# Kernel optimization log

Measured on AMD Instinct MI355X. Metric: run time of the kernel, lower is better.

The kernel has to match this reference:

```python
import jax, jax.numpy as jnp
import numpy as np


def setup_inputs() -> dict:
    key = jax.random.key(0)
    k1, k2, k3 = jax.random.split(key, 3)
    B, T, D, Uh = 64, 256, 1024, 1024
    x = jax.random.normal(k1, (B, T, D), dtype=jnp.float32)
    W = jax.random.normal(k2, (D, 4 * Uh), dtype=jnp.float32) * 0.02
    U = jax.random.normal(k3, (Uh, 4 * Uh), dtype=jnp.float32) * 0.02
    b = jnp.zeros((4 * Uh,), dtype=jnp.float32)
    return {"x": x, "W": W, "U": U, "b": b}


def _lstm(x, W, U, b):
    # Keras LSTM, inference mode (dropout inactive). Gate order: i, f, c, o.
    B = x.shape[0]
    units = U.shape[0]
    # Precompute input projection for all timesteps: [B,T,4U] -> scan over T.
    xz = jnp.einsum('btd,dg->btg', x, W) + b
    xz = jnp.swapaxes(xz, 0, 1)  # [T,B,4U]

    def step(carry, xz_t):
        h, c = carry
        z = xz_t + h @ U  # [B,4U]
        zi, zf, zg, zo = jnp.split(z, 4, axis=-1)
        i = jax.nn.sigmoid(zi)
        f = jax.nn.sigmoid(zf)
        g = jnp.tanh(zg)
        o = jax.nn.sigmoid(zo)
        c_new = f * c + i * g
        h_new = o * jnp.tanh(c_new)
        return (h_new, c_new), h_new

    h0 = jnp.zeros((B, units), dtype=x.dtype)
    c0 = jnp.zeros((B, units), dtype=x.dtype)
    _, hs = jax.lax.scan(step, (h0, c0), xz)  # hs: [T,B,U]
    return jnp.swapaxes(hs, 0, 1)  # [B,T,U] (return_sequences=True)


def reference(x, W, U, b):
    return _lstm(x, W, U, b)
```

## Files before the change

### kernel.cpp

```cpp
#include <hip/hip_runtime.h>
#include <cstdint>
#include <cstddef>

typedef __attribute__((ext_vector_type(8))) short short8;
typedef __attribute__((ext_vector_type(4))) short short4v;
typedef __attribute__((ext_vector_type(4))) float f32x4;
typedef __attribute__((ext_vector_type(4))) int int4v;

static constexpr int B_ = 64, T_ = 256, D_ = 1024, NH = 1024, NG = 4096;
static constexpr int NBLK = 64;
static constexpr int LDS_BYTES = 131072 + 64 * 68 * 4;
static constexpr int GEMM_LDS = 128 * 264 * 2;
static constexpr uint64_t DLY_TICKS = 50;

__device__ __forceinline__ short f2bs(float f) {
  union { float f; uint32_t u; } cv; cv.f = f;
  uint32_t u = cv.u;
  uint32_t r = (u + 0x7fffu + ((u >> 16) & 1u)) >> 16;
  return (short)(uint16_t)r;
}
__device__ __forceinline__ float bs2f(short s) {
  union { uint32_t u; float f; } cv; cv.u = ((uint32_t)(uint16_t)s) << 16; return cv.f;
}
__device__ __forceinline__ float fsigm(float x) {
  return __builtin_amdgcn_rcpf(1.f + __expf(-x));
}
__device__ __forceinline__ float ftanh(float x) {
  return 1.f - 2.f * __builtin_amdgcn_rcpf(__expf(2.f * x) + 1.f);
}
__device__ __forceinline__ uint64_t rtclock() {
  uint64_t v;
  asm volatile("s_memrealtime %0\n\ts_waitcnt lgkmcnt(0)" : "=s"(v));
  return v;
}

__global__ __launch_bounds__(512, 1) void xz_gemm(const float* __restrict__ x,
                                                  const float* __restrict__ W,
                                                  const float* __restrict__ bias,
                                                  short* __restrict__ xzT)
{
  constexpr int BM = 256, BN = 256, BK = 32;
  extern __shared__ char gsm[];
  short* As = (short*)gsm;
  short* Bs = (short*)(gsm + 16384);
  short* Cs = (short*)gsm;

  const int tid  = threadIdx.x;
  const int lane = tid & 63, wave = tid >> 6;
  const int wm = (wave >> 2) * 128, wn = (wave & 3) * 64;
  const int fr = lane & 15, kg = lane >> 4;
  const int bm = blockIdx.x * BM, bn = blockIdx.y * BN;

  f32x4 acc[8][4] = {};

  for (int k0 = 0; k0 < D_; k0 += BK) {
    {
      const int r0 = tid >> 3, kq = (tid & 7) * 4;
      #pragma unroll
      for (int it = 0; it < 4; ++it) {
        const int row = r0 + it * 64;
        const float4 v = *reinterpret_cast<const float4*>(&x[(size_t)(bm + row) * D_ + k0 + kq]);
        short4v s; s.x = f2bs(v.x); s.y = f2bs(v.y); s.z = f2bs(v.z); s.w = f2bs(v.w);
        *reinterpret_cast<short4v*>(&As[row * 32 + kq]) = s;
      }
    }
    {
      const int kr0 = tid >> 6, nq = (tid & 63) * 4;
      #pragma unroll
      for (int it = 0; it < 4; ++it) {
        const int krow = kr0 + it * 8;
        const float4 v = *reinterpret_cast<const float4*>(&W[(size_t)(k0 + krow) * NG + bn + nq]);
        short4v s; s.x = f2bs(v.x); s.y = f2bs(v.y); s.z = f2bs(v.z); s.w = f2bs(v.w);
        *reinterpret_cast<short4v*>(&Bs[krow * 256 + nq]) = s;
      }
    }
    __syncthreads();

    short8 af[8];
    #pragma unroll
    for (int mi = 0; mi < 8; ++mi)
      af[mi] = *reinterpret_cast<const short8*>(&As[(wm + mi * 16 + fr) * 32 + kg * 8]);
    #pragma unroll
    for (int ni = 0; ni < 4; ++ni) {
      short8 bf;
      #pragma unroll
      for (int j = 0; j < 8; ++j) bf[j] = Bs[(kg * 8 + j) * 256 + wn + ni * 16 + fr];
      #pragma unroll
      for (int mi = 0; mi < 8; ++mi)
        acc[mi][ni] = __builtin_amdgcn_mfma_f32_16x16x32_bf16(af[mi], bf, acc[mi][ni], 0, 0, 0);
    }
    __syncthreads();
  }

  const int fq = lane >> 4;
  const int b   = blockIdx.x;
  const int g   = bn >> 10;
  const int rb0 = (bn & 1023) >> 4;
  #pragma unroll
  for (int hp = 0; hp < 2; ++hp) {
    __syncthreads();
    if ((wave >> 2) == hp) {
      #pragma unroll
      for (int ni = 0; ni < 4; ++ni) {
        const int col = wn + ni * 16 + fr;
        const float bv = bias[bn + col];
        #pragma unroll
        for (int mi = 0; mi < 8; ++mi) {
          const int rowl = mi * 16 + fq * 4;
          #pragma unroll
          for (int r = 0; r < 4; ++r)
            Cs[(rowl + r) * 264 + col] = f2bs(acc[mi][ni][r] + bv);
        }
      }
    }
    __syncthreads();
    #pragma unroll
    for (int it = 0; it < 4; ++it) {
      const int cid = it * 512 + tid;
      const int tl = cid >> 4, rbi = cid & 15;
      const int t = hp * 128 + tl;
      short* dst = xzT + ((size_t)((rb0 + rbi) * 256 + t) * 64 + b) * 64 + g * 16;
      const short8 v0 = *reinterpret_cast<const short8*>(&Cs[tl * 264 + rbi * 16]);
      const short8 v1 = *reinterpret_cast<const short8*>(&Cs[tl * 264 + rbi * 16 + 8]);
      *reinterpret_cast<short8*>(dst)     = v0;
      *reinterpret_cast<short8*>(dst + 8) = v1;
    }
  }
}

#define WAITV(N) do { asm volatile("s_waitcnt vmcnt(" #N ")" ::: "memory"); \
                      __builtin_amdgcn_sched_barrier(0); } while (0)

#define HL2(B0, B1, VO) \
  asm volatile("global_load_dwordx4 %0, %2, %3 sc0 sc1\n\t" \
               "global_load_dwordx4 %1, %2, %3 offset:16 sc0 sc1" \
               : "=&v"(B0), "=&v"(B1) : "v"(VO), "s"(hpv) : "memory")

#define ISSUE_A { _Pragma("unroll") \
  for (int K = 0; K < 8; ++K) HL2(bufA[2*K], bufA[2*K+1], voff0 + K * 8192); }
#define ISSUE_B { _Pragma("unroll") \
  for (int K = 0; K < 8; ++K) HL2(bufB[2*K], bufB[2*K+1], voff0 + 65536 + K * 8192); }

#define CHECKBUF(BUF) { _Pragma("unroll") \
  for (int i = 0; i < 16; ++i) { \
    bad |= ((uint32_t)BUF[i][0] ^ tgw); bad |= ((uint32_t)BUF[i][1] ^ tgw); \
    bad |= ((uint32_t)BUF[i][2] ^ tgw); bad |= ((uint32_t)BUF[i][3] ^ tgw); \
  } bad &= 0xFFFF0000u; }

#define MFMA_SUB(BUF, KB) { _Pragma("unroll") \
  for (int K = 0; K < 8; ++K) { \
    int4v pk; \
    pk[0] = (BUF[2*K][0]   & 0xFFFF) | (BUF[2*K][1]   << 16); \
    pk[1] = (BUF[2*K][2]   & 0xFFFF) | (BUF[2*K][3]   << 16); \
    pk[2] = (BUF[2*K+1][0] & 0xFFFF) | (BUF[2*K+1][1] << 16); \
    pk[3] = (BUF[2*K+1][2] & 0xFFFF) | (BUF[2*K+1][3] << 16); \
    const short8 fa = __builtin_bit_cast(short8, pk); \
    const int ksAbs = kh * 16 + (KB) + K; \
    _Pragma("unroll") \
    for (int nt = 0; nt < 4; ++nt) { \
      const short8 fb = *reinterpret_cast<const short8*>(&Us[((ksAbs*4 + kg)*64 + nt*16 + fr)*8]); \
      acc[nt] = __builtin_amdgcn_mfma_f32_16x16x32_bf16(fa, fb, acc[nt], 0, 0, 0); \
    } \
  } }

__global__ __launch_bounds__(512, 2) void lstm_persist(const short* __restrict__ xzT,
                                                       const float* __restrict__ U,
                                                       uint32_t* __restrict__ h0buf,
                                                       uint32_t* __restrict__ h1buf,
                                                       float* __restrict__ out)
{
  extern __shared__ char smem[];
  short* Us  = (short*)smem;
  float* zsm = (float*)(smem + 131072);

  const int tid  = threadIdx.x;
  const int lane = tid & 63, wave = tid >> 6;
  const int bid  = blockIdx.x;
  const int u0   = bid * 16;
  const int fr = lane & 15, kg = lane >> 4;
  const int mt = wave & 3;
  const int kh = wave >> 2;
  const int gb = tid >> 3, gup = tid & 7;

  for (int idx = tid; idx < 1024 * 64; idx += 512) {
    const int k = idx >> 6, c = idx & 63;
    Us[((k >> 3) * 64 + c) * 8 + (k & 7)] =
        f2bs(U[(size_t)k * NG + (c >> 4) * NH + u0 + (c & 15)]);
  }
  float creg0 = 0.f, creg1 = 0.f;
  const int voff0 = kh * 131072 + kg * 2048 + mt * 512 + fr * 32;
  const int pks = bid >> 1;
  const int pkg = ((bid & 1) << 1) + (gup >> 2);
  const int pj  = (2 * gup) & 7;
  const int pidx = ((pks * 4 + pkg) * 64 + gb) * 8 + pj;
  __syncthreads();
  uint64_t rt0 = rtclock();

  for (int t = 0; t < T_; ++t) {
    const uint32_t* __restrict__ hpv = (t & 1) ? h0buf : h1buf;
    uint32_t* __restrict__ hnx       = (t & 1) ? h1buf : h0buf;

    int xzw[4];
    {
      const short* xb = xzT + (((size_t)bid * 256 + t) * 64 + gb) * 64;
      #pragma unroll
      for (int g = 0; g < 4; ++g)
        xzw[g] = *reinterpret_cast<const int*>(xb + g * 16 + 2 * gup);
    }

    f32x4 acc[4] = {};
    if (t > 0) {
      const uint32_t tgw = (uint32_t)t << 16;
      int4v bufA[16], bufB[16];
      while ((uint64_t)(rtclock() - rt0) < DLY_TICKS)
        __builtin_amdgcn_s_sleep(1);
      ISSUE_A; ISSUE_B;
      WAITV(16);
      for (;;) {
        uint32_t bad = 0; CHECKBUF(bufA);
        if (__all(bad == 0)) break;
        __builtin_amdgcn_s_sleep(4);
        ISSUE_A; WAITV(0);
      }
      MFMA_SUB(bufA, 0);
      WAITV(0);
      for (;;) {
        uint32_t bad = 0; CHECKBUF(bufB);
        if (__all(bad == 0)) break;
        __builtin_amdgcn_s_sleep(4);
        ISSUE_B; WAITV(0);
      }
      MFMA_SUB(bufB, 8);

      if (kh == 1) {
        #pragma unroll
        for (int nt = 0; nt < 4; ++nt)
          #pragma unroll
          for (int r = 0; r < 4; ++r)
            zsm[(mt * 16 + kg * 4 + r) * 68 + nt * 16 + fr] = acc[nt][r];
      }
      __syncthreads();
      if (kh == 0) {
        #pragma unroll
        for (int nt = 0; nt < 4; ++nt)
          #pragma unroll
          for (int r = 0; r < 4; ++r)
            zsm[(mt * 16 + kg * 4 + r) * 68 + nt * 16 + fr] += acc[nt][r];
      }
      __syncthreads();
    }

    {
      float z[4][2];
      #pragma unroll
      for (int g = 0; g < 4; ++g) {
        z[g][0] = bs2f((short)(xzw[g] & 0xFFFF));
        z[g][1] = bs2f((short)(((uint32_t)xzw[g]) >> 16));
        if (t > 0) {
          const float2 zz = *reinterpret_cast<const float2*>(&zsm[gb * 68 + g * 16 + 2 * gup]);
          z[g][0] += zz.x; z[g][1] += zz.y;
        }
      }
      float hh0, hh1;
      {
        const float ig = fsigm(z[0][0]), fg = fsigm(z[1][0]);
        const float gg = ftanh(z[2][0]), og = fsigm(z[3][0]);
        creg0 = fg * creg0 + ig * gg;  hh0 = og * ftanh(creg0);
      }
      {
        const float ig = fsigm(z[0][1]), fg = fsigm(z[1][1]);
        const float gg = ftanh(z[2][1]), og = fsigm(z[3][1]);
        creg1 = fg * creg1 + ig * gg;  hh1 = og * ftanh(creg1);
      }
      if (t < T_ - 1) {
        const uint32_t tgp = (uint32_t)(t + 1) << 16;
        const uint64_t hw64 =
            (uint64_t)(tgp | (uint32_t)(uint16_t)f2bs(hh0)) |
            ((uint64_t)(tgp | (uint32_t)(uint16_t)f2bs(hh1)) << 32);
        (void)__hip_atomic_exchange((uint64_t*)(hnx + pidx), hw64,
                                    __ATOMIC_RELAXED, __HIP_MEMORY_SCOPE_AGENT);
      }
      rt0 = rtclock();
      float2 o; o.x = hh0; o.y = hh1;
      *reinterpret_cast<float2*>(&out[((size_t)gb * T_ + t) * NH + u0 + 2 * gup]) = o;
    }
    __builtin_amdgcn_s_barrier();
  }
}

extern "C" void kernel_launch(void* const* d_in, const int* in_sizes, int n_in,
                              void* d_out, int out_size, void* d_ws, size_t ws_size,
                              hipStream_t stream) {
  const float* x    = (const float*)d_in[0];
  const float* W    = (const float*)d_in[1];
  const float* U    = (const float*)d_in[2];
  const float* bias = (const float*)d_in[3];
  float* out = (float*)d_out;
  char* ws = (char*)d_ws;

  short*    xzT = (short*)ws;
  uint32_t* hA  = (uint32_t*)(ws + 134217728);
  uint32_t* hB  = (uint32_t*)(ws + 134217728 + 262144);

  hipMemsetAsync(ws + 134217728, 0, 524288, stream);

  hipFuncSetAttribute((const void*)xz_gemm,
                      hipFuncAttributeMaxDynamicSharedMemorySize, GEMM_LDS);
  xz_gemm<<<dim3(64, 16), 512, GEMM_LDS, stream>>>(x, W, bias, xzT);

  hipFuncSetAttribute((const void*)lstm_persist,
                      hipFuncAttributeMaxDynamicSharedMemorySize, LDS_BYTES);
  lstm_persist<<<dim3(NBLK), dim3(512), LDS_BYTES, stream>>>(xzT, U, hA, hB, out);
}
```

Before: 1.954 ms.

## Rewrite recurrent LSTM kernel with int8 weights and hidden state across 256 blocks

Replaces the 64-block persistent recurrence with a 256-block kernel. Work is split into 8 batch groups times 32 unit slices. U is quantized to int8 with per-column scales and h to int8, so the per-step matmul uses i8 MFMA with a smaller A operand. The xz layout and the h exchange buffers are reorganized for the new decomposition, and the realtime-clock delay is replaced by retry polling with cache-bypass escalation. This aims to cut per-step latency and spread the work across more CUs, at the cost of int8 quantization error on both weights and the hidden state.

```diff
diff --git a/kernel.cpp b/kernel.cpp
--- a/kernel.cpp
+++ b/kernel.cpp
@@ -6,12 +6,11 @@
 typedef __attribute__((ext_vector_type(4))) short short4v;
 typedef __attribute__((ext_vector_type(4))) float f32x4;
 typedef __attribute__((ext_vector_type(4))) int int4v;
+typedef __attribute__((ext_vector_type(2))) int int2v;
 
 static constexpr int B_ = 64, T_ = 256, D_ = 1024, NH = 1024, NG = 4096;
-static constexpr int NBLK = 64;
-static constexpr int LDS_BYTES = 131072 + 64 * 68 * 4;
 static constexpr int GEMM_LDS = 128 * 264 * 2;
-static constexpr uint64_t DLY_TICKS = 50;
+static constexpr int REC_LDS = 131072 + 4352 + 512 + 2048;
 
 __device__ __forceinline__ short f2bs(float f) {
   union { float f; uint32_t u; } cv; cv.f = f;
@@ -27,11 +26,6 @@
 }
 __device__ __forceinline__ float ftanh(float x) {
   return 1.f - 2.f * __builtin_amdgcn_rcpf(__expf(2.f * x) + 1.f);
-}
-__device__ __forceinline__ uint64_t rtclock() {
-  uint64_t v;
-  asm volatile("s_memrealtime %0\n\ts_waitcnt lgkmcnt(0)" : "=s"(v));
-  return v;
 }
 
 __global__ __launch_bounds__(512, 1) void xz_gemm(const float* __restrict__ x,
@@ -93,9 +87,9 @@
   }
 
   const int fq = lane >> 4;
-  const int b   = blockIdx.x;
-  const int g   = bn >> 10;
-  const int rb0 = (bn & 1023) >> 4;
+  const int bglob = blockIdx.x;
+  const int gg    = bn >> 10;
+  const int utile = bn & 1023;
   #pragma unroll
   for (int hp = 0; hp < 2; ++hp) {
     __syncthreads();
@@ -119,7 +113,11 @@
       const int cid = it * 512 + tid;
       const int tl = cid >> 4, rbi = cid & 15;
       const int t = hp * 128 + tl;
-      short* dst = xzT + ((size_t)((rb0 + rbi) * 256 + t) * 64 + b) * 64 + g * 16;
+      const int ul = utile + rbi * 16;
+      const int slc = ul >> 5, ub = ul & 31;
+      const int bidr = slc * 8 + (bglob >> 3);
+      short* dst = xzT + (size_t)bidr * 262144 + (size_t)t * 1024
+                 + (bglob & 7) * 128 + gg * 32 + ub;
       const short8 v0 = *reinterpret_cast<const short8*>(&Cs[tl * 264 + rbi * 16]);
       const short8 v1 = *reinterpret_cast<const short8*>(&Cs[tl * 264 + rbi * 16 + 8]);
       *reinterpret_cast<short8*>(dst)     = v0;
@@ -131,158 +129,158 @@
 #define WAITV(N) do { asm volatile("s_waitcnt vmcnt(" #N ")" ::: "memory"); \
                       __builtin_amdgcn_sched_barrier(0); } while (0)
 
-#define HL2(B0, B1, VO) \
-  asm volatile("global_load_dwordx4 %0, %2, %3 sc0 sc1\n\t" \
-               "global_load_dwordx4 %1, %2, %3 offset:16 sc0 sc1" \
-               : "=&v"(B0), "=&v"(B1) : "v"(VO), "s"(hpv) : "memory")
-
-#define ISSUE_A { _Pragma("unroll") \
-  for (int K = 0; K < 8; ++K) HL2(bufA[2*K], bufA[2*K+1], voff0 + K * 8192); }
-#define ISSUE_B { _Pragma("unroll") \
-  for (int K = 0; K < 8; ++K) HL2(bufB[2*K], bufB[2*K+1], voff0 + 65536 + K * 8192); }
-
-#define CHECKBUF(BUF) { _Pragma("unroll") \
+#define H1F(B0, VO) \
+  asm volatile("global_load_dwordx4 %0, %1, %2 sc0" \
+               : "=&v"(B0) : "v"(VO), "s"(hpv) : "memory")
+#define H1S(B0, VO) \
+  asm volatile("global_load_dwordx4 %0, %1, %2 sc0 sc1" \
+               : "=&v"(B0) : "v"(VO), "s"(hpv) : "memory")
+
+#define ISSUE16F(BUF, BASE) { _Pragma("unroll") \
+  for (int K = 0; K < 16; ++K) H1F(BUF[K], voff0 + (BASE) + K * 1024); }
+#define ISSUE16S(BUF, BASE) { _Pragma("unroll") \
+  for (int K = 0; K < 16; ++K) H1S(BUF[K], voff0 + (BASE) + K * 1024); }
+
+#define CHECK16(BUF) { uint32_t bb = 0; _Pragma("unroll") \
   for (int i = 0; i < 16; ++i) { \
-    bad |= ((uint32_t)BUF[i][0] ^ tgw); bad |= ((uint32_t)BUF[i][1] ^ tgw); \
-    bad |= ((uint32_t)BUF[i][2] ^ tgw); bad |= ((uint32_t)BUF[i][3] ^ tgw); \
-  } bad &= 0xFFFF0000u; }
-
-#define MFMA_SUB(BUF, KB) { _Pragma("unroll") \
-  for (int K = 0; K < 8; ++K) { \
-    int4v pk; \
-    pk[0] = (BUF[2*K][0]   & 0xFFFF) | (BUF[2*K][1]   << 16); \
-    pk[1] = (BUF[2*K][2]   & 0xFFFF) | (BUF[2*K][3]   << 16); \
-    pk[2] = (BUF[2*K+1][0] & 0xFFFF) | (BUF[2*K+1][1] << 16); \
-    pk[3] = (BUF[2*K+1][2] & 0xFFFF) | (BUF[2*K+1][3] << 16); \
-    const short8 fa = __builtin_bit_cast(short8, pk); \
-    const int ksAbs = kh * 16 + (KB) + K; \
-    _Pragma("unroll") \
-    for (int nt = 0; nt < 4; ++nt) { \
-      const short8 fb = *reinterpret_cast<const short8*>(&Us[((ksAbs*4 + kg)*64 + nt*16 + fr)*8]); \
-      acc[nt] = __builtin_amdgcn_mfma_f32_16x16x32_bf16(fa, fb, acc[nt], 0, 0, 0); \
-    } \
+    bb |= ((uint32_t)BUF[i][0] ^ tgw); bb |= ((uint32_t)BUF[i][1] ^ tgw); \
+    bb |= ((uint32_t)BUF[i][2] ^ tgw); bb |= ((uint32_t)BUF[i][3] ^ tgw); \
+  } bad = frlt8 ? (bb & 0xFFFF0000u) : 0u; }
+
+#define MFMA16(BUF, KB) { _Pragma("unroll") \
+  for (int K = 0; K < 16; ++K) { \
+    int2v ad; \
+    ad[0] = (BUF[K][0] & 0xFFFF) | ((BUF[K][1] & 0xFFFF) << 16); \
+    ad[1] = (BUF[K][2] & 0xFFFF) | ((BUF[K][3] & 0xFFFF) << 16); \
+    const long long a64 = frlt8 ? __builtin_bit_cast(long long, ad) : 0ll; \
+    const int ksAbs = (KB) + K; \
+    const long long b64 = *reinterpret_cast<const long long*>( \
+        &Us[(size_t)(((ksAbs * 4 + kg) * 128 + wave * 16 + fr)) * 8]); \
+    acc = __builtin_amdgcn_mfma_i32_16x16x32_i8(a64, b64, acc, 0, 0, 0); \
   } }
 
-__global__ __launch_bounds__(512, 2) void lstm_persist(const short* __restrict__ xzT,
-                                                       const float* __restrict__ U,
-                                                       uint32_t* __restrict__ h0buf,
-                                                       uint32_t* __restrict__ h1buf,
-                                                       float* __restrict__ out)
+__global__ __launch_bounds__(512, 2) void lstm_rec(
+    const short* __restrict__ xzT, const float* __restrict__ U,
+    uint32_t* __restrict__ h0buf, uint32_t* __restrict__ h1buf,
+    float* __restrict__ out)
 {
   extern __shared__ char smem[];
-  short* Us  = (short*)smem;
-  float* zsm = (float*)(smem + 131072);
+  char*  Us   = smem;
+  float* zsm  = (float*)(smem + 131072);
+  float* scl  = (float*)(smem + 131072 + 4352);
+  float* pmax = (float*)(smem + 131072 + 4864);
 
   const int tid  = threadIdx.x;
   const int lane = tid & 63, wave = tid >> 6;
   const int bid  = blockIdx.x;
-  const int u0   = bid * 16;
+  const int g    = bid & 7;
+  const int sl   = bid >> 3;
   const int fr = lane & 15, kg = lane >> 4;
-  const int mt = wave & 3;
-  const int kh = wave >> 2;
-  const int gb = tid >> 3, gup = tid & 7;
-
-  for (int idx = tid; idx < 1024 * 64; idx += 512) {
-    const int k = idx >> 6, c = idx & 63;
-    Us[((k >> 3) * 64 + c) * 8 + (k & 7)] =
-        f2bs(U[(size_t)k * NG + (c >> 4) * NH + u0 + (c & 15)]);
-  }
-  float creg0 = 0.f, creg1 = 0.f;
-  const int voff0 = kh * 131072 + kg * 2048 + mt * 512 + fr * 32;
-  const int pks = bid >> 1;
-  const int pkg = ((bid & 1) << 1) + (gup >> 2);
-  const int pj  = (2 * gup) & 7;
-  const int pidx = ((pks * 4 + pkg) * 64 + gb) * 8 + pj;
+  const bool frlt8 = (fr < 8);
+
+  {
+    const int c = tid & 127, q = tid >> 7;
+    const float* up = U + (size_t)(q * 256) * NG + (c >> 5) * NH + sl * 32 + (c & 31);
+    float m = 1e-30f;
+    for (int k = 0; k < 256; ++k) m = fmaxf(m, fabsf(up[(size_t)k * NG]));
+    pmax[q * 128 + c] = m;
+  }
   __syncthreads();
-  uint64_t rt0 = rtclock();
+  if (tid < 128)
+    scl[tid] = fmaxf(fmaxf(pmax[tid], pmax[128 + tid]),
+                     fmaxf(pmax[256 + tid], pmax[384 + tid]));
+  __syncthreads();
+  for (int idx = tid; idx < 131072; idx += 512) {
+    const int k = idx >> 7, c = idx & 127;
+    const float v = U[(size_t)k * NG + (c >> 5) * NH + sl * 32 + (c & 31)];
+    Us[(size_t)(((k >> 5) * 4 + ((k >> 3) & 3)) * 128 + c) * 8 + (k & 7)] =
+        (char)(int)rintf(v * (127.f / scl[c]));
+  }
+  const float sdiv = scl[wave * 16 + fr] * (1.f / 16129.f);
+  float creg = 0.f;
+  const int voff0 = kg * 256 + fr * 16;
+  __syncthreads();
 
   for (int t = 0; t < T_; ++t) {
-    const uint32_t* __restrict__ hpv = (t & 1) ? h0buf : h1buf;
-    uint32_t* __restrict__ hnx       = (t & 1) ? h1buf : h0buf;
-
-    int xzw[4];
-    {
-      const short* xb = xzT + (((size_t)bid * 256 + t) * 64 + gb) * 64;
-      #pragma unroll
-      for (int g = 0; g < 4; ++g)
-        xzw[g] = *reinterpret_cast<const int*>(xb + g * 16 + 2 * gup);
-    }
-
-    f32x4 acc[4] = {};
+    const uint32_t* hpv = ((t & 1) ? h0buf : h1buf) + g * 8192;
+    uint32_t*       hnx = ((t & 1) ? h1buf : h0buf) + g * 8192;
+
+    float xzv0 = 0.f, xzv1 = 0.f, xzv2 = 0.f, xzv3 = 0.f;
+    if (tid < 256) {
+      const short* xb = xzT + (size_t)bid * 262144 + (size_t)t * 1024
+                      + (tid >> 5) * 128 + (tid & 31);
+      xzv0 = bs2f(xb[0]);  xzv1 = bs2f(xb[32]);
+      xzv2 = bs2f(xb[64]); xzv3 = bs2f(xb[96]);
+    }
+
+    int4v acc = {};
     if (t > 0) {
       const uint32_t tgw = (uint32_t)t << 16;
       int4v bufA[16], bufB[16];
-      while ((uint64_t)(rtclock() - rt0) < DLY_TICKS)
-        __builtin_amdgcn_s_sleep(1);
-      ISSUE_A; ISSUE_B;
+      if (frlt8) { ISSUE16F(bufA, 0); ISSUE16F(bufB, 16384); }
       WAITV(16);
-      for (;;) {
-        uint32_t bad = 0; CHECKBUF(bufA);
-        if (__all(bad == 0)) break;
-        __builtin_amdgcn_s_sleep(4);
-        ISSUE_A; WAITV(0);
-      }
-      MFMA_SUB(bufA, 0);
+      {
+        int tries = 0; uint32_t bad;
+        for (;;) {
+          CHECK16(bufA);
+          if (__all(bad == 0)) break;
+          __builtin_amdgcn_s_sleep(1);
+          ++tries;
+          if (frlt8) { if (tries < 6) { ISSUE16F(bufA, 0); } else { ISSUE16S(bufA, 0); } }
+          WAITV(0);
+        }
+      }
+      MFMA16(bufA, 0);
       WAITV(0);
-      for (;;) {
-        uint32_t bad = 0; CHECKBUF(bufB);
-        if (__all(bad == 0)) break;
-        __builtin_amdgcn_s_sleep(4);
-        ISSUE_B; WAITV(0);
-      }
-      MFMA_SUB(bufB, 8);
-
-      if (kh == 1) {
+      {
+        int tries = 0; uint32_t bad;
+        for (;;) {
+          CHECK16(bufB);
+          if (__all(bad == 0)) break;
+          __builtin_amdgcn_s_sleep(1);
+          ++tries;
+          if (frlt8) { if (tries < 6) { ISSUE16F(bufB, 16384); } else { ISSUE16S(bufB, 16384); } }
+          WAITV(0);
+        }
+      }
+      MFMA16(bufB, 16);
+
+      if (lane < 32) {
+        const int rowb = (lane >> 4) * 4;
         #pragma unroll
-        for (int nt = 0; nt < 4; ++nt)
-          #pragma unroll
-          for (int r = 0; r < 4; ++r)
-            zsm[(mt * 16 + kg * 4 + r) * 68 + nt * 16 + fr] = acc[nt][r];
-      }
-      __syncthreads();
-      if (kh == 0) {
-        #pragma unroll
-        for (int nt = 0; nt < 4; ++nt)
-          #pragma unroll
-          for (int r = 0; r < 4; ++r)
-            zsm[(mt * 16 + kg * 4 + r) * 68 + nt * 16 + fr] += acc[nt][r];
-      }
-      __syncthreads();
-    }
-
-    {
-      float z[4][2];
-      #pragma unroll
-      for (int g = 0; g < 4; ++g) {
-        z[g][0] = bs2f((short)(xzw[g] & 0xFFFF));
-        z[g][1] = bs2f((short)(((uint32_t)xzw[g]) >> 16));
-        if (t > 0) {
-          const float2 zz = *reinterpret_cast<const float2*>(&zsm[gb * 68 + g * 16 + 2 * gup]);
-          z[g][0] += zz.x; z[g][1] += zz.y;
+        for (int r = 0; r < 4; ++r)
+          zsm[(rowb + r) * 132 + wave * 16 + fr] = (float)acc[r] * sdiv;
+      }
+    }
+    __syncthreads();
+
+    if (tid < 256) {
+      const int b = tid >> 5, uu = tid & 31;
+      float z0 = xzv0, z1 = xzv1, z2 = xzv2, z3 = xzv3;
+      if (t > 0) {
+        z0 += zsm[b * 132 + uu];
+        z1 += zsm[b * 132 + 32 + uu];
+        z2 += zsm[b * 132 + 64 + uu];
+        z3 += zsm[b * 132 + 96 + uu];
+      }
+      const float ig = fsigm(z0), fg = fsigm(z1);
+      const float gg2 = ftanh(z2), og = fsigm(z3);
+      creg = fg * creg + ig * gg2;
+      const float hh = og * ftanh(creg);
+
+      if (t < T_ - 1) {
+        const int q = (int)rintf(hh * 127.f);
+        const int qp = __shfl_xor(q, 1);
+        if (!(uu & 1)) {
+          const uint32_t word = ((uint32_t)(t + 1) << 16)
+                              | (((uint32_t)qp & 0xFFu) << 8) | ((uint32_t)q & 0xFFu);
+          uint32_t* hp = hnx + ((sl * 4 + (uu >> 3)) * 16 + b) * 4 + ((uu >> 1) & 3);
+          asm volatile("global_store_dword %0, %1, off sc0\n\t"
+                       "global_store_dword %0, %1, off sc0 sc1"
+                       :: "v"(hp), "v"(word) : "memory");
         }
       }
-      float hh0, hh1;
-      {
-        const float ig = fsigm(z[0][0]), fg = fsigm(z[1][0]);
-        const float gg = ftanh(z[2][0]), og = fsigm(z[3][0]);
-        creg0 = fg * creg0 + ig * gg;  hh0 = og * ftanh(creg0);
-      }
-      {
-        const float ig = fsigm(z[0][1]), fg = fsigm(z[1][1]);
-        const float gg = ftanh(z[2][1]), og = fsigm(z[3][1]);
-        creg1 = fg * creg1 + ig * gg;  hh1 = og * ftanh(creg1);
-      }
-      if (t < T_ - 1) {
-        const uint32_t tgp = (uint32_t)(t + 1) << 16;
-        const uint64_t hw64 =
-            (uint64_t)(tgp | (uint32_t)(uint16_t)f2bs(hh0)) |
-            ((uint64_t)(tgp | (uint32_t)(uint16_t)f2bs(hh1)) << 32);
-        (void)__hip_atomic_exchange((uint64_t*)(hnx + pidx), hw64,
-                                    __ATOMIC_RELAXED, __HIP_MEMORY_SCOPE_AGENT);
-      }
-      rt0 = rtclock();
-      float2 o; o.x = hh0; o.y = hh1;
-      *reinterpret_cast<float2*>(&out[((size_t)gb * T_ + t) * NH + u0 + 2 * gup]) = o;
+      out[((size_t)(8 * g + b) * 256 + t) * 1024 + 32 * sl + uu] = hh;
     }
     __builtin_amdgcn_s_barrier();
   }
@@ -308,7 +306,7 @@
                       hipFuncAttributeMaxDynamicSharedMemorySize, GEMM_LDS);
   xz_gemm<<<dim3(64, 16), 512, GEMM_LDS, stream>>>(x, W, bias, xzT);
 
-  hipFuncSetAttribute((const void*)lstm_persist,
-                      hipFuncAttributeMaxDynamicSharedMemorySize, LDS_BYTES);
-  lstm_persist<<<dim3(NBLK), dim3(512), LDS_BYTES, stream>>>(xzT, U, hA, hB, out);
-}
+  hipFuncSetAttribute((const void*)lstm_rec,
+                      hipFuncAttributeMaxDynamicSharedMemorySize, REC_LDS);
+  lstm_rec<<<dim3(256), 512, REC_LDS, stream>>>(xzT, U, hA, hB, out);
+}
```

After: 3.598 ms. 1.84x slower.
